# Kernel optimization log

Hardware: AMD Instinct MI355X
Metric: run time of the kernel (lower is better)

## Reference

```python
import jax, jax.numpy as jnp
import numpy as np

H = 64  # hidden_dim


def setup_inputs() -> dict:
    key = jax.random.key(0)
    ks = jax.random.split(key, 6)
    B, S, F = 256, 512, 128
    C = 100
    # small init scale keeps sigmoid/tanh out of saturation (like torch default init)
    return {
        "x": jax.random.normal(ks[0], (B, S, F), dtype=jnp.float32),
        "W_x2h": jax.random.normal(ks[1], (3 * H, F), dtype=jnp.float32) * 0.05,
        "W_h2h": jax.random.normal(ks[2], (3 * H, H), dtype=jnp.float32) * 0.05,
        "W1": jax.random.normal(ks[3], (512, S * H), dtype=jnp.float32) * 0.02,
        "W2": jax.random.normal(ks[4], (256, 512), dtype=jnp.float32) * 0.05,
        "W3": jax.random.normal(ks[5], (C, 256), dtype=jnp.float32) * 0.05,
    }


def reference(x, W_x2h, W_h2h, W1, W2, W3):
    B, S, F = x.shape
    # Precompute input-to-hidden gates for all timesteps in one GEMM: (B,S,3H)
    gx_all = jnp.einsum("bsf,gf->bsg", x, W_x2h)

    def step(h, gx):
        gh = h @ W_h2h.T  # (B, 3H)
        i_r, i_i, i_n = jnp.split(gx, 3, axis=1)
        h_r, h_i, h_n = jnp.split(gh, 3, axis=1)
        resetgate = jax.nn.sigmoid(i_r + h_r)
        inputgate = jax.nn.sigmoid(i_i + h_i)
        newgate = jnp.tanh(i_n + resetgate * h_n)
        h_new = newgate + inputgate * (h - newgate)
        return h_new, h_new

    h0 = jnp.zeros((B, H), dtype=x.dtype)
    _, outs = jax.lax.scan(step, h0, jnp.swapaxes(gx_all, 0, 1))  # outs: (S,B,H)
    out = jnp.swapaxes(outs, 0, 1).reshape(B, S * H)  # stack along dim 1, then flatten

    out = jax.nn.relu(out @ W1.T)
    out = jax.nn.relu(out @ W2.T)
    out = out @ W3.T
    return jax.nn.softmax(out, axis=1)
```

## Files before the change

kernel.cpp:

```cpp
#include <hip/hip_runtime.h>


constexpr int B = 256, S = 512, F = 128, H = 64, G = 192, C = 100;
constexpr int N1 = 512;
constexpr int SCHUNK = 128, NCHUNK = 4;
constexpr int K1 = S * H;

typedef __attribute__((ext_vector_type(8))) __bf16 bf16x8;
typedef __attribute__((ext_vector_type(4))) float f32x4;

__device__ __forceinline__ unsigned short f2bf(float f) {
  unsigned int u = __float_as_uint(f);
  unsigned int r = (u + 0x7FFFu + ((u >> 16) & 1u)) >> 16;
  return (unsigned short)r;
}
__device__ __forceinline__ float bf2f(unsigned short s) {
  return __uint_as_float((unsigned int)s << 16);
}
__device__ __forceinline__ float sigm_fast(float x) {
  float e = __builtin_amdgcn_exp2f(-1.4426950408889634f * x);
  return __builtin_amdgcn_rcpf(1.f + e);
}
__device__ __forceinline__ float tanh_fast(float x) {
  float e = __builtin_amdgcn_exp2f(2.8853900817779268f * x);
  return 1.f - 2.f * __builtin_amdgcn_rcpf(1.f + e);
}
__device__ __forceinline__ float quad_add(float v) {
  int y = __builtin_amdgcn_update_dpp(0, __float_as_int(v), 0xB1, 0xF, 0xF, true);
  float s = v + __int_as_float(y);
  int z = __builtin_amdgcn_update_dpp(0, __float_as_int(s), 0x4E, 0xF, 0xF, true);
  return s + __int_as_float(z);
}

__global__ void k_convW(const float* __restrict__ Wx, unsigned short* __restrict__ Wh_hi,
                        unsigned short* __restrict__ Wh_lo) {
  int el = blockIdx.x * 256 + threadIdx.x;
  float v = Wx[el];
  unsigned short hi = f2bf(v);
  Wh_hi[el] = hi;
  Wh_lo[el] = f2bf(v - bf2f(hi));
}

__global__ __launch_bounds__(256, 1) void k_gemm_gx(const float* __restrict__ x,
                                                    const unsigned short* __restrict__ Whp,
                                                    const unsigned short* __restrict__ Wlp,
                                                    float* __restrict__ gx, int sc) {
  __shared__ unsigned short Ah[128 * 32];
  __shared__ unsigned short Al[128 * 32];
  __shared__ unsigned short Bh[192 * 32];
  __shared__ unsigned short Bl[192 * 32];
  const int t = threadIdx.x;
  const int b = blockIdx.x;
  const int w = t >> 6, l = t & 63;
  const int wm = w >> 1, wn = w & 1;
  const float* arow = x + ((size_t)b * S + (size_t)sc * SCHUNK) * F;

  f32x4 acc[4][6] = {};

  const int ar_ = t >> 1, ahh = t & 1;
  for (int kc = 0; kc < 4; kc++) {
    const int k0 = kc * 32;
    {
      const float* sp = arow + (size_t)ar_ * F + k0 + ahh * 16;
      float fv[16];
#pragma unroll
      for (int c = 0; c < 4; c++) {
        float4 v = *(const float4*)(sp + c * 4);
        fv[c * 4 + 0] = v.x; fv[c * 4 + 1] = v.y; fv[c * 4 + 2] = v.z; fv[c * 4 + 3] = v.w;
      }
      unsigned short hi[16], lo[16];
#pragma unroll
      for (int e = 0; e < 16; e++) {
        hi[e] = f2bf(fv[e]);
        lo[e] = f2bf(fv[e] - bf2f(hi[e]));
      }
#pragma unroll
      for (int half = 0; half < 2; half++) {
        int cq = ahh * 2 + half;
        int sq = cq ^ (ar_ & 3);
        unsigned short* dh = &Ah[ar_ * 32 + sq * 8];
        unsigned short* dl = &Al[ar_ * 32 + sq * 8];
#pragma unroll
        for (int e = 0; e < 8; e++) {
          dh[e] = hi[half * 8 + e];
          dl[e] = lo[half * 8 + e];
        }
      }
    }
    if (t < 192) {
#pragma unroll
      for (int cq = 0; cq < 4; cq++) {
        int sq = cq ^ (t & 3);
        *(uint4*)&Bh[t * 32 + sq * 8] = *(const uint4*)(Whp + (size_t)t * F + k0 + cq * 8);
        *(uint4*)&Bl[t * 32 + sq * 8] = *(const uint4*)(Wlp + (size_t)t * F + k0 + cq * 8);
      }
    }
    __syncthreads();
    bf16x8 bhf[6], blf[6];
#pragma unroll
    for (int nf = 0; nf < 6; nf++) {
      int rowb = wn * 96 + nf * 16 + (l & 15);
      int sq = (l >> 4) ^ (rowb & 3);
      bhf[nf] = *(const bf16x8*)&Bh[rowb * 32 + sq * 8];
      blf[nf] = *(const bf16x8*)&Bl[rowb * 32 + sq * 8];
    }
#pragma unroll
    for (int mf = 0; mf < 4; mf++) {
      int rowa = wm * 64 + mf * 16 + (l & 15);
      int sq = (l >> 4) ^ (rowa & 3);
      bf16x8 ah = *(const bf16x8*)&Ah[rowa * 32 + sq * 8];
      bf16x8 al = *(const bf16x8*)&Al[rowa * 32 + sq * 8];
#pragma unroll
      for (int nf = 0; nf < 6; nf++) {
        acc[mf][nf] = __builtin_amdgcn_mfma_f32_16x16x32_bf16(ah, bhf[nf], acc[mf][nf], 0, 0, 0);
        acc[mf][nf] = __builtin_amdgcn_mfma_f32_16x16x32_bf16(al, bhf[nf], acc[mf][nf], 0, 0, 0);
        acc[mf][nf] = __builtin_amdgcn_mfma_f32_16x16x32_bf16(ah, blf[nf], acc[mf][nf], 0, 0, 0);
      }
    }
    __syncthreads();
  }
#pragma unroll
  for (int mf = 0; mf < 4; mf++) {
#pragma unroll
    for (int nf = 0; nf < 6; nf++) {
      int m = wm * 64 + mf * 16 + (l >> 4) * 4;
      int n = wn * 96 + nf * 16 + (l & 15);
      float* dst = gx + ((size_t)b * SCHUNK + m) * G + n;
#pragma unroll
      for (int r = 0; r < 4; r++) dst[(size_t)r * G] = acc[mf][nf][r];
    }
  }
}

__global__ __launch_bounds__(256, 1) void k_scan(const float* __restrict__ gx,
                                                 const float* __restrict__ Wh,
                                                 unsigned short* __restrict__ outh,
                                                 unsigned short* __restrict__ outl,
                                                 float* __restrict__ hst, int sc) {
  __shared__ float h_s[2][64];
  const int t = threadIdx.x;
  const int w = t >> 6, l = t & 63;
  const int j = (w << 4) | (l >> 2);
  const int q = l & 3;
  const int b = blockIdx.x;

  float Wr[16], Wi[16], Wn[16];
  {
    const float* p0 = Wh + (size_t)j * H + q * 16;
    const float* p1 = Wh + (size_t)(64 + j) * H + q * 16;
    const float* p2 = Wh + (size_t)(128 + j) * H + q * 16;
#pragma unroll
    for (int c = 0; c < 4; c++) {
      float4 v0 = *(const float4*)(p0 + c * 4);
      float4 v1 = *(const float4*)(p1 + c * 4);
      float4 v2 = *(const float4*)(p2 + c * 4);
      Wr[c * 4 + 0] = v0.x; Wr[c * 4 + 1] = v0.y; Wr[c * 4 + 2] = v0.z; Wr[c * 4 + 3] = v0.w;
      Wi[c * 4 + 0] = v1.x; Wi[c * 4 + 1] = v1.y; Wi[c * 4 + 2] = v1.z; Wi[c * 4 + 3] = v1.w;
      Wn[c * 4 + 0] = v2.x; Wn[c * 4 + 1] = v2.y; Wn[c * 4 + 2] = v2.z; Wn[c * 4 + 3] = v2.w;
    }
  }
  float h_own;
  if (sc == 0) {
    h_own = 0.f;
    if (t < 64) h_s[0][t] = 0.f;
  } else {
    h_own = hst[b * H + j];
    if (t < 64) h_s[0][t] = hst[b * H + t];
  }
  asm volatile("s_waitcnt lgkmcnt(0)\n\ts_barrier" ::: "memory");

  const float* gxb = gx + (size_t)b * SCHUNK * G;
  float gr0 = gxb[j], gi0 = gxb[64 + j], gn0 = gxb[128 + j];
  float gr1 = gxb[G + j], gi1 = gxb[G + 64 + j], gn1 = gxb[G + 128 + j];
  unsigned short* poh = outh + (size_t)b * K1 + (size_t)sc * SCHUNK * H + j;
  unsigned short* pol = outl + (size_t)b * K1 + (size_t)sc * SCHUNK * H + j;

  int cur = 0;
  for (int sl = 0; sl < SCHUNK; sl++) {
    const float* hb = &h_s[cur][q * 16];
    float4 ha = *(const float4*)(hb);
    float4 hc = *(const float4*)(hb + 4);
    float4 hd = *(const float4*)(hb + 8);
    float4 he = *(const float4*)(hb + 12);
    int pf = (sl + 2 < SCHUNK) ? sl + 2 : SCHUNK - 1;
    const float* gp = gxb + (size_t)pf * G;
    float grn = gp[j], gin = gp[64 + j], gnn = gp[128 + j];

    float ar, ai, an;
    ar = Wr[0] * ha.x; ai = Wi[0] * ha.x; an = Wn[0] * ha.x;
    ar = fmaf(Wr[1], ha.y, ar); ai = fmaf(Wi[1], ha.y, ai); an = fmaf(Wn[1], ha.y, an);
    ar = fmaf(Wr[2], ha.z, ar); ai = fmaf(Wi[2], ha.z, ai); an = fmaf(Wn[2], ha.z, an);
    ar = fmaf(Wr[3], ha.w, ar); ai = fmaf(Wi[3], ha.w, ai); an = fmaf(Wn[3], ha.w, an);
    ar = fmaf(Wr[4], hc.x, ar); ai = fmaf(Wi[4], hc.x, ai); an = fmaf(Wn[4], hc.x, an);
    ar = fmaf(Wr[5], hc.y, ar); ai = fmaf(Wi[5], hc.y, ai); an = fmaf(Wn[5], hc.y, an);
    ar = fmaf(Wr[6], hc.z, ar); ai = fmaf(Wi[6], hc.z, ai); an = fmaf(Wn[6], hc.z, an);
    ar = fmaf(Wr[7], hc.w, ar); ai = fmaf(Wi[7], hc.w, ai); an = fmaf(Wn[7], hc.w, an);
    ar = fmaf(Wr[8], hd.x, ar); ai = fmaf(Wi[8], hd.x, ai); an = fmaf(Wn[8], hd.x, an);
    ar = fmaf(Wr[9], hd.y, ar); ai = fmaf(Wi[9], hd.y, ai); an = fmaf(Wn[9], hd.y, an);
    ar = fmaf(Wr[10], hd.z, ar); ai = fmaf(Wi[10], hd.z, ai); an = fmaf(Wn[10], hd.z, an);
    ar = fmaf(Wr[11], hd.w, ar); ai = fmaf(Wi[11], hd.w, ai); an = fmaf(Wn[11], hd.w, an);
    ar = fmaf(Wr[12], he.x, ar); ai = fmaf(Wi[12], he.x, ai); an = fmaf(Wn[12], he.x, an);
    ar = fmaf(Wr[13], he.y, ar); ai = fmaf(Wi[13], he.y, ai); an = fmaf(Wn[13], he.y, an);
    ar = fmaf(Wr[14], he.z, ar); ai = fmaf(Wi[14], he.z, ai); an = fmaf(Wn[14], he.z, an);
    ar = fmaf(Wr[15], he.w, ar); ai = fmaf(Wi[15], he.w, ai); an = fmaf(Wn[15], he.w, an);

    ar = quad_add(ar);
    ai = quad_add(ai);
    an = quad_add(an);

    float rr = sigm_fast(ar + gr0);
    float ii = sigm_fast(ai + gi0);
    float na = gn0 + rr * an;
    float th = tanh_fast(na);
    h_own = th + ii * (h_own - th);

    int nxt = cur ^ 1;
    if (q == 0) {
      h_s[nxt][j] = h_own;
      unsigned short hh2 = f2bf(h_own);
      poh[(size_t)sl * H] = hh2;
      pol[(size_t)sl * H] = f2bf(h_own - bf2f(hh2));
    }
    gr0 = gr1; gi0 = gi1; gn0 = gn1;
    gr1 = grn; gi1 = gin; gn1 = gnn;
    asm volatile("s_waitcnt lgkmcnt(0)\n\ts_barrier" ::: "memory");
    cur = nxt;
  }
  if (q == 0) hst[b * H + j] = h_own;
}

__global__ __launch_bounds__(256, 1) void k_fc1(const unsigned short* __restrict__ Ahp,
                                                const unsigned short* __restrict__ Alp,
                                                const float* __restrict__ W1,
                                                float* __restrict__ psum, int KCH) {
  __shared__ unsigned short Ah[256 * 32];
  __shared__ unsigned short Al[256 * 32];
  __shared__ unsigned short Bh[128 * 32];
  __shared__ unsigned short Bl[128 * 32];
  const int t = threadIdx.x;
  const int ntile = blockIdx.x & 3;
  const int ks = blockIdx.x >> 2;
  const int k0b = ks * KCH;
  const int w = t >> 6, l = t & 63;
  const int wm = w >> 1, wn = w & 1;

  f32x4 acc[8][4] = {};

  const int br = t >> 1, bhh = t & 1;
  const float* bsrc = W1 + (size_t)(ntile * 128 + br) * K1 + bhh * 16;
  const int nkc = KCH >> 5;

  for (int kc = 0; kc < nkc; kc++) {
    const int k0 = k0b + kc * 32;
#pragma unroll
    for (int i = 0; i < 4; i++) {
      int slot = t + i * 256;
      int row = slot >> 2, sq = slot & 3;
      int cq = sq ^ (row & 3);
      const uint4* sh = (const uint4*)(Ahp + (size_t)row * K1 + k0 + cq * 8);
      const uint4* sl2 = (const uint4*)(Alp + (size_t)row * K1 + k0 + cq * 8);
      *(uint4*)&Ah[row * 32 + sq * 8] = *sh;
      *(uint4*)&Al[row * 32 + sq * 8] = *sl2;
    }
    {
      const float* sp = bsrc + k0;
      float fv[16];
#pragma unroll
      for (int c = 0; c < 4; c++) {
        float4 v = *(const float4*)(sp + c * 4);
        fv[c * 4 + 0] = v.x; fv[c * 4 + 1] = v.y; fv[c * 4 + 2] = v.z; fv[c * 4 + 3] = v.w;
      }
      unsigned short hi[16], lo[16];
#pragma unroll
      for (int e = 0; e < 16; e++) {
        hi[e] = f2bf(fv[e]);
        lo[e] = f2bf(fv[e] - bf2f(hi[e]));
      }
#pragma unroll
      for (int half = 0; half < 2; half++) {
        int cq = bhh * 2 + half;
        int sq = cq ^ (br & 3);
        unsigned short* dh = &Bh[br * 32 + sq * 8];
        unsigned short* dl = &Bl[br * 32 + sq * 8];
#pragma unroll
        for (int e = 0; e < 8; e++) {
          dh[e] = hi[half * 8 + e];
          dl[e] = lo[half * 8 + e];
        }
      }
    }
    __syncthreads();
    bf16x8 bhf[4], blf[4];
#pragma unroll
    for (int nf = 0; nf < 4; nf++) {
      int rowb = wn * 64 + nf * 16 + (l & 15);
      int sq = (l >> 4) ^ (rowb & 3);
      bhf[nf] = *(const bf16x8*)&Bh[rowb * 32 + sq * 8];
      blf[nf] = *(const bf16x8*)&Bl[rowb * 32 + sq * 8];
    }
#pragma unroll
    for (int mf = 0; mf < 8; mf++) {
      int rowa = wm * 128 + mf * 16 + (l & 15);
      int sq = (l >> 4) ^ (rowa & 3);
      bf16x8 ah = *(const bf16x8*)&Ah[rowa * 32 + sq * 8];
      bf16x8 al = *(const bf16x8*)&Al[rowa * 32 + sq * 8];
#pragma unroll
      for (int nf = 0; nf < 4; nf++) {
        acc[mf][nf] = __builtin_amdgcn_mfma_f32_16x16x32_bf16(ah, bhf[nf], acc[mf][nf], 0, 0, 0);
        acc[mf][nf] = __builtin_amdgcn_mfma_f32_16x16x32_bf16(al, bhf[nf], acc[mf][nf], 0, 0, 0);
        acc[mf][nf] = __builtin_amdgcn_mfma_f32_16x16x32_bf16(ah, blf[nf], acc[mf][nf], 0, 0, 0);
      }
    }
    __syncthreads();
  }
#pragma unroll
  for (int mf = 0; mf < 8; mf++) {
#pragma unroll
    for (int nf = 0; nf < 4; nf++) {
      int m = wm * 128 + mf * 16 + (l >> 4) * 4;
      int n = ntile * 128 + wn * 64 + nf * 16 + (l & 15);
      float* dst = psum + ((size_t)ks * 256 + m) * N1 + n;
#pragma unroll
      for (int r = 0; r < 4; r++) dst[(size_t)r * N1] = acc[mf][nf][r];
    }
  }
}

__global__ void k_red(const float* __restrict__ psum, float* __restrict__ out1, int KS) {
  int i = (blockIdx.x * 256 + threadIdx.x) * 4;
  float4 s = make_float4(0.f, 0.f, 0.f, 0.f);
  for (int ks = 0; ks < KS; ks++) {
    float4 v = *(const float4*)(psum + (size_t)ks * (B * N1) + i);
    s.x += v.x; s.y += v.y; s.z += v.z; s.w += v.w;
  }
  *(float4*)(out1 + i) = s;
}

__global__ __launch_bounds__(256, 1) void k_tail(const float* __restrict__ out1,
                                                 const float* __restrict__ W2,
                                                 const float* __restrict__ W3,
                                                 float* __restrict__ dout) {
  __shared__ float o1[N1];
  __shared__ float o2[256];
  __shared__ float lg[128];
  const int tid = threadIdx.x;
  const int b = blockIdx.x;
  {
    float2 v = *(const float2*)(out1 + (size_t)b * N1 + tid * 2);
    o1[tid * 2 + 0] = fmaxf(v.x, 0.f);
    o1[tid * 2 + 1] = fmaxf(v.y, 0.f);
  }
  __syncthreads();
  {
    const float* w2r = W2 + (size_t)tid * N1;
    float a0 = 0, a1 = 0, a2 = 0, a3 = 0;
#pragma unroll 4
    for (int k = 0; k < N1; k += 4) {
      float4 ov = *(const float4*)(o1 + k);
      float4 wv = *(const float4*)(w2r + k);
      a0 = fmaf(ov.x, wv.x, a0);
      a1 = fmaf(ov.y, wv.y, a1);
      a2 = fmaf(ov.z, wv.z, a2);
      a3 = fmaf(ov.w, wv.w, a3);
    }
    o2[tid] = fmaxf((a0 + a1) + (a2 + a3), 0.f);
  }
  __syncthreads();
  if (tid < C) {
    const float* w3r = W3 + (size_t)tid * 256;
    float a0 = 0, a1 = 0, a2 = 0, a3 = 0;
#pragma unroll 4
    for (int k = 0; k < 256; k += 4) {
      float4 ov = *(const float4*)(o2 + k);
      float4 wv = *(const float4*)(w3r + k);
      a0 = fmaf(ov.x, wv.x, a0);
      a1 = fmaf(ov.y, wv.y, a1);
      a2 = fmaf(ov.z, wv.z, a2);
      a3 = fmaf(ov.w, wv.w, a3);
    }
    lg[tid] = (a0 + a1) + (a2 + a3);
  }
  __syncthreads();
  if (tid < 64) {
    float v0 = lg[tid];
    float v1 = (tid + 64 < C) ? lg[tid + 64] : -3.0e38f;
    float m = fmaxf(v0, v1);
#pragma unroll
    for (int off = 32; off > 0; off >>= 1) m = fmaxf(m, __shfl_xor(m, off, 64));
    float e0 = __expf(v0 - m);
    float e1 = (tid + 64 < C) ? __expf(v1 - m) : 0.f;
    float ssum = e0 + e1;
#pragma unroll
    for (int off = 32; off > 0; off >>= 1) ssum += __shfl_xor(ssum, off, 64);
    float inv = 1.f / ssum;
    dout[(size_t)b * C + tid] = e0 * inv;
    if (tid + 64 < C) dout[(size_t)b * C + tid + 64] = e1 * inv;
  }
}

extern "C" void kernel_launch(void* const* d_in, const int* in_sizes, int n_in,
                              void* d_out, int out_size, void* d_ws, size_t ws_size,
                              hipStream_t stream) {
  (void)in_sizes; (void)n_in; (void)out_size;
  const float* x = (const float*)d_in[0];
  const float* Wx = (const float*)d_in[1];
  const float* Wh = (const float*)d_in[2];
  const float* W1 = (const float*)d_in[3];
  const float* W2 = (const float*)d_in[4];
  const float* W3 = (const float*)d_in[5];
  float* ws = (float*)d_ws;

  const int KS = (ws_size >= 110ull * 1024 * 1024) ? 64 : 32;
  const int KCH = K1 / KS;

  const size_t gx_f = (size_t)B * SCHUNK * G;
  const size_t psum_f = (size_t)KS * B * N1;
  const size_t region0 = (psum_f > gx_f) ? psum_f : gx_f;

  float* gx = ws;
  float* psum = ws;
  unsigned short* gouth = (unsigned short*)(ws + region0);
  unsigned short* goutl = gouth + (size_t)B * K1;
  float* out1 = (float*)(goutl + (size_t)B * K1);
  float* hst = out1 + (size_t)B * N1;
  unsigned short* Wxh = (unsigned short*)(hst + (size_t)B * H);
  unsigned short* Wxl = Wxh + (size_t)G * F;

  k_convW<<<dim3((G * F) / 256), dim3(256), 0, stream>>>(Wx, Wxh, Wxl);
  for (int sc = 0; sc < NCHUNK; sc++) {
    k_gemm_gx<<<dim3(B), dim3(256), 0, stream>>>(x, Wxh, Wxl, gx, sc);
    k_scan<<<dim3(B), dim3(256), 0, stream>>>(gx, Wh, gouth, goutl, hst, sc);
  }
  k_fc1<<<dim3(4 * KS), dim3(256), 0, stream>>>(gouth, goutl, W1, psum, KCH);
  k_red<<<dim3(128), dim3(256), 0, stream>>>(psum, out1, KS);
  k_tail<<<dim3(B), dim3(256), 0, stream>>>(out1, W2, W3, (float*)d_out);
}
```

Baseline: 488.9 us.

## Fuse input GEMM into GRU scan kernel and use atomic split-K for FC1

The per-chunk input-projection GEMM and the recurrent scan are merged into one persistent kernel. Each block computes its gate pre-activations into a shared-memory buffer of about 96 KB and then runs the scan over all four chunks. This drops eight launches, the global gx round trip and the hidden-state save and restore between chunks. FC1 moves to 512-thread blocks with a fixed split-K of 64 and a block-index swizzle, and it accumulates with atomicAdd into a zeroed output instead of writing partial sums and running a separate reduction. In exchange the scan block needs a large LDS allocation, loads the A and B operands straight from global memory without staging, and the FC1 result becomes order-nondeterministic.

```diff
diff --git a/kernel.cpp b/kernel.cpp
--- a/kernel.cpp
+++ b/kernel.cpp
@@ -7,7 +7,13 @@
 constexpr int K1 = S * H;
 
 typedef __attribute__((ext_vector_type(8))) __bf16 bf16x8;
+typedef __attribute__((ext_vector_type(8))) short s16x8;
 typedef __attribute__((ext_vector_type(4))) float f32x4;
+
+union BFU {
+  s16x8 s;
+  bf16x8 b;
+};
 
 __device__ __forceinline__ unsigned short f2bf(float f) {
   unsigned int u = __float_as_uint(f);
@@ -41,110 +47,23 @@
   Wh_lo[el] = f2bf(v - bf2f(hi));
 }
 
-__global__ __launch_bounds__(256, 1) void k_gemm_gx(const float* __restrict__ x,
-                                                    const unsigned short* __restrict__ Whp,
-                                                    const unsigned short* __restrict__ Wlp,
-                                                    float* __restrict__ gx, int sc) {
-  __shared__ unsigned short Ah[128 * 32];
-  __shared__ unsigned short Al[128 * 32];
-  __shared__ unsigned short Bh[192 * 32];
-  __shared__ unsigned short Bl[192 * 32];
-  const int t = threadIdx.x;
-  const int b = blockIdx.x;
-  const int w = t >> 6, l = t & 63;
-  const int wm = w >> 1, wn = w & 1;
-  const float* arow = x + ((size_t)b * S + (size_t)sc * SCHUNK) * F;
-
-  f32x4 acc[4][6] = {};
-
-  const int ar_ = t >> 1, ahh = t & 1;
-  for (int kc = 0; kc < 4; kc++) {
-    const int k0 = kc * 32;
-    {
-      const float* sp = arow + (size_t)ar_ * F + k0 + ahh * 16;
-      float fv[16];
-#pragma unroll
-      for (int c = 0; c < 4; c++) {
-        float4 v = *(const float4*)(sp + c * 4);
-        fv[c * 4 + 0] = v.x; fv[c * 4 + 1] = v.y; fv[c * 4 + 2] = v.z; fv[c * 4 + 3] = v.w;
-      }
-      unsigned short hi[16], lo[16];
-#pragma unroll
-      for (int e = 0; e < 16; e++) {
-        hi[e] = f2bf(fv[e]);
-        lo[e] = f2bf(fv[e] - bf2f(hi[e]));
-      }
-#pragma unroll
-      for (int half = 0; half < 2; half++) {
-        int cq = ahh * 2 + half;
-        int sq = cq ^ (ar_ & 3);
-        unsigned short* dh = &Ah[ar_ * 32 + sq * 8];
-        unsigned short* dl = &Al[ar_ * 32 + sq * 8];
-#pragma unroll
-        for (int e = 0; e < 8; e++) {
-          dh[e] = hi[half * 8 + e];
-          dl[e] = lo[half * 8 + e];
-        }
-      }
-    }
-    if (t < 192) {
-#pragma unroll
-      for (int cq = 0; cq < 4; cq++) {
-        int sq = cq ^ (t & 3);
-        *(uint4*)&Bh[t * 32 + sq * 8] = *(const uint4*)(Whp + (size_t)t * F + k0 + cq * 8);
-        *(uint4*)&Bl[t * 32 + sq * 8] = *(const uint4*)(Wlp + (size_t)t * F + k0 + cq * 8);
-      }
-    }
-    __syncthreads();
-    bf16x8 bhf[6], blf[6];
-#pragma unroll
-    for (int nf = 0; nf < 6; nf++) {
-      int rowb = wn * 96 + nf * 16 + (l & 15);
-      int sq = (l >> 4) ^ (rowb & 3);
-      bhf[nf] = *(const bf16x8*)&Bh[rowb * 32 + sq * 8];
-      blf[nf] = *(const bf16x8*)&Bl[rowb * 32 + sq * 8];
-    }
-#pragma unroll
-    for (int mf = 0; mf < 4; mf++) {
-      int rowa = wm * 64 + mf * 16 + (l & 15);
-      int sq = (l >> 4) ^ (rowa & 3);
-      bf16x8 ah = *(const bf16x8*)&Ah[rowa * 32 + sq * 8];
-      bf16x8 al = *(const bf16x8*)&Al[rowa * 32 + sq * 8];
-#pragma unroll
-      for (int nf = 0; nf < 6; nf++) {
-        acc[mf][nf] = __builtin_amdgcn_mfma_f32_16x16x32_bf16(ah, bhf[nf], acc[mf][nf], 0, 0, 0);
-        acc[mf][nf] = __builtin_amdgcn_mfma_f32_16x16x32_bf16(al, bhf[nf], acc[mf][nf], 0, 0, 0);
-        acc[mf][nf] = __builtin_amdgcn_mfma_f32_16x16x32_bf16(ah, blf[nf], acc[mf][nf], 0, 0, 0);
-      }
-    }
-    __syncthreads();
-  }
-#pragma unroll
-  for (int mf = 0; mf < 4; mf++) {
-#pragma unroll
-    for (int nf = 0; nf < 6; nf++) {
-      int m = wm * 64 + mf * 16 + (l >> 4) * 4;
-      int n = wn * 96 + nf * 16 + (l & 15);
-      float* dst = gx + ((size_t)b * SCHUNK + m) * G + n;
-#pragma unroll
-      for (int r = 0; r < 4; r++) dst[(size_t)r * G] = acc[mf][nf][r];
-    }
-  }
-}
-
-__global__ __launch_bounds__(256, 1) void k_scan(const float* __restrict__ gx,
-                                                 const float* __restrict__ Wh,
-                                                 unsigned short* __restrict__ outh,
-                                                 unsigned short* __restrict__ outl,
-                                                 float* __restrict__ hst, int sc) {
+__global__ __launch_bounds__(256, 1) void k_fused(const float* __restrict__ x,
+                                                  const unsigned short* __restrict__ Whp,
+                                                  const unsigned short* __restrict__ Wlp,
+                                                  const float* __restrict__ Wh,
+                                                  unsigned short* __restrict__ outh,
+                                                  unsigned short* __restrict__ outl) {
+  __shared__ float gxl[SCHUNK * G];
   __shared__ float h_s[2][64];
   const int t = threadIdx.x;
   const int w = t >> 6, l = t & 63;
+  const int b = blockIdx.x;
+  const int wm = w >> 1, wn = w & 1;
+  const int lm = l & 15, lk = l >> 4;
   const int j = (w << 4) | (l >> 2);
   const int q = l & 3;
-  const int b = blockIdx.x;
-
-  float Wr[16], Wi[16], Wn[16];
+
+  float Wr[16], Wi[16], Wn_[16];
   {
     const float* p0 = Wh + (size_t)j * H + q * 16;
     const float* p1 = Wh + (size_t)(64 + j) * H + q * 16;
@@ -156,152 +75,179 @@
       float4 v2 = *(const float4*)(p2 + c * 4);
       Wr[c * 4 + 0] = v0.x; Wr[c * 4 + 1] = v0.y; Wr[c * 4 + 2] = v0.z; Wr[c * 4 + 3] = v0.w;
       Wi[c * 4 + 0] = v1.x; Wi[c * 4 + 1] = v1.y; Wi[c * 4 + 2] = v1.z; Wi[c * 4 + 3] = v1.w;
-      Wn[c * 4 + 0] = v2.x; Wn[c * 4 + 1] = v2.y; Wn[c * 4 + 2] = v2.z; Wn[c * 4 + 3] = v2.w;
-    }
-  }
-  float h_own;
-  if (sc == 0) {
-    h_own = 0.f;
-    if (t < 64) h_s[0][t] = 0.f;
-  } else {
-    h_own = hst[b * H + j];
-    if (t < 64) h_s[0][t] = hst[b * H + t];
-  }
-  asm volatile("s_waitcnt lgkmcnt(0)\n\ts_barrier" ::: "memory");
-
-  const float* gxb = gx + (size_t)b * SCHUNK * G;
-  float gr0 = gxb[j], gi0 = gxb[64 + j], gn0 = gxb[128 + j];
-  float gr1 = gxb[G + j], gi1 = gxb[G + 64 + j], gn1 = gxb[G + 128 + j];
-  unsigned short* poh = outh + (size_t)b * K1 + (size_t)sc * SCHUNK * H + j;
-  unsigned short* pol = outl + (size_t)b * K1 + (size_t)sc * SCHUNK * H + j;
-
+      Wn_[c * 4 + 0] = v2.x; Wn_[c * 4 + 1] = v2.y; Wn_[c * 4 + 2] = v2.z; Wn_[c * 4 + 3] = v2.w;
+    }
+  }
+  float h_own = 0.f;
+  if (t < 64) h_s[0][t] = 0.f;
   int cur = 0;
-  for (int sl = 0; sl < SCHUNK; sl++) {
-    const float* hb = &h_s[cur][q * 16];
-    float4 ha = *(const float4*)(hb);
-    float4 hc = *(const float4*)(hb + 4);
-    float4 hd = *(const float4*)(hb + 8);
-    float4 he = *(const float4*)(hb + 12);
-    int pf = (sl + 2 < SCHUNK) ? sl + 2 : SCHUNK - 1;
-    const float* gp = gxb + (size_t)pf * G;
-    float grn = gp[j], gin = gp[64 + j], gnn = gp[128 + j];
-
-    float ar, ai, an;
-    ar = Wr[0] * ha.x; ai = Wi[0] * ha.x; an = Wn[0] * ha.x;
-    ar = fmaf(Wr[1], ha.y, ar); ai = fmaf(Wi[1], ha.y, ai); an = fmaf(Wn[1], ha.y, an);
-    ar = fmaf(Wr[2], ha.z, ar); ai = fmaf(Wi[2], ha.z, ai); an = fmaf(Wn[2], ha.z, an);
-    ar = fmaf(Wr[3], ha.w, ar); ai = fmaf(Wi[3], ha.w, ai); an = fmaf(Wn[3], ha.w, an);
-    ar = fmaf(Wr[4], hc.x, ar); ai = fmaf(Wi[4], hc.x, ai); an = fmaf(Wn[4], hc.x, an);
-    ar = fmaf(Wr[5], hc.y, ar); ai = fmaf(Wi[5], hc.y, ai); an = fmaf(Wn[5], hc.y, an);
-    ar = fmaf(Wr[6], hc.z, ar); ai = fmaf(Wi[6], hc.z, ai); an = fmaf(Wn[6], hc.z, an);
-    ar = fmaf(Wr[7], hc.w, ar); ai = fmaf(Wi[7], hc.w, ai); an = fmaf(Wn[7], hc.w, an);
-    ar = fmaf(Wr[8], hd.x, ar); ai = fmaf(Wi[8], hd.x, ai); an = fmaf(Wn[8], hd.x, an);
-    ar = fmaf(Wr[9], hd.y, ar); ai = fmaf(Wi[9], hd.y, ai); an = fmaf(Wn[9], hd.y, an);
-    ar = fmaf(Wr[10], hd.z, ar); ai = fmaf(Wi[10], hd.z, ai); an = fmaf(Wn[10], hd.z, an);
-    ar = fmaf(Wr[11], hd.w, ar); ai = fmaf(Wi[11], hd.w, ai); an = fmaf(Wn[11], hd.w, an);
-    ar = fmaf(Wr[12], he.x, ar); ai = fmaf(Wi[12], he.x, ai); an = fmaf(Wn[12], he.x, an);
-    ar = fmaf(Wr[13], he.y, ar); ai = fmaf(Wi[13], he.y, ai); an = fmaf(Wn[13], he.y, an);
-    ar = fmaf(Wr[14], he.z, ar); ai = fmaf(Wi[14], he.z, ai); an = fmaf(Wn[14], he.z, an);
-    ar = fmaf(Wr[15], he.w, ar); ai = fmaf(Wi[15], he.w, ai); an = fmaf(Wn[15], he.w, an);
-
-    ar = quad_add(ar);
-    ai = quad_add(ai);
-    an = quad_add(an);
-
-    float rr = sigm_fast(ar + gr0);
-    float ii = sigm_fast(ai + gi0);
-    float na = gn0 + rr * an;
-    float th = tanh_fast(na);
-    h_own = th + ii * (h_own - th);
-
-    int nxt = cur ^ 1;
-    if (q == 0) {
-      h_s[nxt][j] = h_own;
-      unsigned short hh2 = f2bf(h_own);
-      poh[(size_t)sl * H] = hh2;
-      pol[(size_t)sl * H] = f2bf(h_own - bf2f(hh2));
-    }
-    gr0 = gr1; gi0 = gi1; gn0 = gn1;
-    gr1 = grn; gi1 = gin; gn1 = gnn;
-    asm volatile("s_waitcnt lgkmcnt(0)\n\ts_barrier" ::: "memory");
-    cur = nxt;
-  }
-  if (q == 0) hst[b * H + j] = h_own;
-}
-
-__global__ __launch_bounds__(256, 1) void k_fc1(const unsigned short* __restrict__ Ahp,
+  __syncthreads();
+
+  unsigned short* poh_b = outh + (size_t)b * K1 + j;
+  unsigned short* pol_b = outl + (size_t)b * K1 + j;
+
+  for (int sc = 0; sc < NCHUNK; sc++) {
+    const float* arow = x + ((size_t)b * S + (size_t)sc * SCHUNK) * F;
+    f32x4 acc[4][6] = {};
+#pragma unroll
+    for (int kc = 0; kc < 4; kc++) {
+      const int k0 = kc * 32;
+      bf16x8 bhf[6], blf[6];
+#pragma unroll
+      for (int nf = 0; nf < 6; nf++) {
+        int g = wn * 96 + nf * 16 + lm;
+        bhf[nf] = *(const bf16x8*)(Whp + (size_t)g * F + k0 + lk * 8);
+        blf[nf] = *(const bf16x8*)(Wlp + (size_t)g * F + k0 + lk * 8);
+      }
+#pragma unroll
+      for (int mf = 0; mf < 4; mf++) {
+        int rowa = wm * 64 + mf * 16 + lm;
+        const float* ap = arow + (size_t)rowa * F + k0 + lk * 8;
+        float4 a0 = *(const float4*)(ap);
+        float4 a1 = *(const float4*)(ap + 4);
+        float av[8] = {a0.x, a0.y, a0.z, a0.w, a1.x, a1.y, a1.z, a1.w};
+        BFU ah, al;
+#pragma unroll
+        for (int e = 0; e < 8; e++) {
+          unsigned short hi = f2bf(av[e]);
+          ah.s[e] = (short)hi;
+          al.s[e] = (short)f2bf(av[e] - bf2f(hi));
+        }
+#pragma unroll
+        for (int nf = 0; nf < 6; nf++) {
+          acc[mf][nf] = __builtin_amdgcn_mfma_f32_16x16x32_bf16(ah.b, bhf[nf], acc[mf][nf], 0, 0, 0);
+          acc[mf][nf] = __builtin_amdgcn_mfma_f32_16x16x32_bf16(al.b, bhf[nf], acc[mf][nf], 0, 0, 0);
+          acc[mf][nf] = __builtin_amdgcn_mfma_f32_16x16x32_bf16(ah.b, blf[nf], acc[mf][nf], 0, 0, 0);
+        }
+      }
+    }
+#pragma unroll
+    for (int mf = 0; mf < 4; mf++)
+#pragma unroll
+      for (int nf = 0; nf < 6; nf++) {
+        int m = wm * 64 + mf * 16 + lk * 4;
+        int n = wn * 96 + nf * 16 + lm;
+#pragma unroll
+        for (int r = 0; r < 4; r++) gxl[(m + r) * G + n] = acc[mf][nf][r];
+      }
+    __syncthreads();
+
+    float gr = gxl[j], gi = gxl[64 + j], gn = gxl[128 + j];
+    for (int sl = 0; sl < SCHUNK; sl++) {
+      const float* hb = &h_s[cur][q * 16];
+      float4 ha = *(const float4*)(hb);
+      float4 hc = *(const float4*)(hb + 4);
+      float4 hd = *(const float4*)(hb + 8);
+      float4 he = *(const float4*)(hb + 12);
+      int np = (sl + 1) & (SCHUNK - 1);
+      float grn = gxl[np * G + j];
+      float gin = gxl[np * G + 64 + j];
+      float gnn = gxl[np * G + 128 + j];
+
+      float ar, ai, an;
+      ar = Wr[0] * ha.x; ai = Wi[0] * ha.x; an = Wn_[0] * ha.x;
+      ar = fmaf(Wr[1], ha.y, ar); ai = fmaf(Wi[1], ha.y, ai); an = fmaf(Wn_[1], ha.y, an);
+      ar = fmaf(Wr[2], ha.z, ar); ai = fmaf(Wi[2], ha.z, ai); an = fmaf(Wn_[2], ha.z, an);
+      ar = fmaf(Wr[3], ha.w, ar); ai = fmaf(Wi[3], ha.w, ai); an = fmaf(Wn_[3], ha.w, an);
+      ar = fmaf(Wr[4], hc.x, ar); ai = fmaf(Wi[4], hc.x, ai); an = fmaf(Wn_[4], hc.x, an);
+      ar = fmaf(Wr[5], hc.y, ar); ai = fmaf(Wi[5], hc.y, ai); an = fmaf(Wn_[5], hc.y, an);
+      ar = fmaf(Wr[6], hc.z, ar); ai = fmaf(Wi[6], hc.z, ai); an = fmaf(Wn_[6], hc.z, an);
+      ar = fmaf(Wr[7], hc.w, ar); ai = fmaf(Wi[7], hc.w, ai); an = fmaf(Wn_[7], hc.w, an);
+      ar = fmaf(Wr[8], hd.x, ar); ai = fmaf(Wi[8], hd.x, ai); an = fmaf(Wn_[8], hd.x, an);
+      ar = fmaf(Wr[9], hd.y, ar); ai = fmaf(Wi[9], hd.y, ai); an = fmaf(Wn_[9], hd.y, an);
+      ar = fmaf(Wr[10], hd.z, ar); ai = fmaf(Wi[10], hd.z, ai); an = fmaf(Wn_[10], hd.z, an);
+      ar = fmaf(Wr[11], hd.w, ar); ai = fmaf(Wi[11], hd.w, ai); an = fmaf(Wn_[11], hd.w, an);
+      ar = fmaf(Wr[12], he.x, ar); ai = fmaf(Wi[12], he.x, ai); an = fmaf(Wn_[12], he.x, an);
+      ar = fmaf(Wr[13], he.y, ar); ai = fmaf(Wi[13], he.y, ai); an = fmaf(Wn_[13], he.y, an);
+      ar = fmaf(Wr[14], he.z, ar); ai = fmaf(Wi[14], he.z, ai); an = fmaf(Wn_[14], he.z, an);
+      ar = fmaf(Wr[15], he.w, ar); ai = fmaf(Wi[15], he.w, ai); an = fmaf(Wn_[15], he.w, an);
+
+      ar = quad_add(ar);
+      ai = quad_add(ai);
+      an = quad_add(an);
+
+      float rr = sigm_fast(ar + gr);
+      float ii = sigm_fast(ai + gi);
+      float na = gn + rr * an;
+      float th = tanh_fast(na);
+      h_own = th + ii * (h_own - th);
+
+      int nxt = cur ^ 1;
+      if (q == 0) {
+        h_s[nxt][j] = h_own;
+        unsigned short hh = f2bf(h_own);
+        size_t so = (size_t)(sc * SCHUNK + sl) * H;
+        poh_b[so] = hh;
+        pol_b[so] = f2bf(h_own - bf2f(hh));
+      }
+      gr = grn; gi = gin; gn = gnn;
+      asm volatile("s_waitcnt lgkmcnt(0)\n\ts_barrier" ::: "memory");
+      cur = nxt;
+    }
+  }
+}
+
+__global__ __launch_bounds__(512, 1) void k_fc1(const unsigned short* __restrict__ Ahp,
                                                 const unsigned short* __restrict__ Alp,
                                                 const float* __restrict__ W1,
-                                                float* __restrict__ psum, int KCH) {
+                                                float* __restrict__ out1) {
   __shared__ unsigned short Ah[256 * 32];
   __shared__ unsigned short Al[256 * 32];
   __shared__ unsigned short Bh[128 * 32];
   __shared__ unsigned short Bl[128 * 32];
   const int t = threadIdx.x;
-  const int ntile = blockIdx.x & 3;
-  const int ks = blockIdx.x >> 2;
-  const int k0b = ks * KCH;
+  const int bid = blockIdx.x;
+  const int v = (bid & 7) * 32 + (bid >> 3);
+  const int ks = v >> 2, ntile = v & 3;
+  const int k0b = ks * 512;
   const int w = t >> 6, l = t & 63;
   const int wm = w >> 1, wn = w & 1;
-
-  f32x4 acc[8][4] = {};
-
-  const int br = t >> 1, bhh = t & 1;
-  const float* bsrc = W1 + (size_t)(ntile * 128 + br) * K1 + bhh * 16;
-  const int nkc = KCH >> 5;
-
-  for (int kc = 0; kc < nkc; kc++) {
+  const int lm = l & 15, lk = l >> 4;
+
+  f32x4 acc[4][4] = {};
+  const int br = t >> 2, qt = t & 3;
+
+  for (int kc = 0; kc < 16; kc++) {
     const int k0 = k0b + kc * 32;
 #pragma unroll
-    for (int i = 0; i < 4; i++) {
-      int slot = t + i * 256;
+    for (int i = 0; i < 2; i++) {
+      int slot = t + i * 512;
       int row = slot >> 2, sq = slot & 3;
       int cq = sq ^ (row & 3);
-      const uint4* sh = (const uint4*)(Ahp + (size_t)row * K1 + k0 + cq * 8);
-      const uint4* sl2 = (const uint4*)(Alp + (size_t)row * K1 + k0 + cq * 8);
-      *(uint4*)&Ah[row * 32 + sq * 8] = *sh;
-      *(uint4*)&Al[row * 32 + sq * 8] = *sl2;
+      *(uint4*)&Ah[row * 32 + sq * 8] = *(const uint4*)(Ahp + (size_t)row * K1 + k0 + cq * 8);
+      *(uint4*)&Al[row * 32 + sq * 8] = *(const uint4*)(Alp + (size_t)row * K1 + k0 + cq * 8);
     }
     {
-      const float* sp = bsrc + k0;
-      float fv[16];
-#pragma unroll
-      for (int c = 0; c < 4; c++) {
-        float4 v = *(const float4*)(sp + c * 4);
-        fv[c * 4 + 0] = v.x; fv[c * 4 + 1] = v.y; fv[c * 4 + 2] = v.z; fv[c * 4 + 3] = v.w;
-      }
-      unsigned short hi[16], lo[16];
-#pragma unroll
-      for (int e = 0; e < 16; e++) {
-        hi[e] = f2bf(fv[e]);
-        lo[e] = f2bf(fv[e] - bf2f(hi[e]));
-      }
-#pragma unroll
-      for (int half = 0; half < 2; half++) {
-        int cq = bhh * 2 + half;
-        int sq = cq ^ (br & 3);
-        unsigned short* dh = &Bh[br * 32 + sq * 8];
-        unsigned short* dl = &Bl[br * 32 + sq * 8];
-#pragma unroll
-        for (int e = 0; e < 8; e++) {
-          dh[e] = hi[half * 8 + e];
-          dl[e] = lo[half * 8 + e];
-        }
-      }
+      const float* sp = W1 + (size_t)(ntile * 128 + br) * K1 + k0 + qt * 8;
+      float4 v0 = *(const float4*)(sp);
+      float4 v1 = *(const float4*)(sp + 4);
+      float fv[8] = {v0.x, v0.y, v0.z, v0.w, v1.x, v1.y, v1.z, v1.w};
+      unsigned int hp[4], lp[4];
+#pragma unroll
+      for (int e = 0; e < 4; e++) {
+        unsigned short h0 = f2bf(fv[2 * e]), h1 = f2bf(fv[2 * e + 1]);
+        unsigned short l0 = f2bf(fv[2 * e] - bf2f(h0));
+        unsigned short l1 = f2bf(fv[2 * e + 1] - bf2f(h1));
+        hp[e] = (unsigned int)h0 | ((unsigned int)h1 << 16);
+        lp[e] = (unsigned int)l0 | ((unsigned int)l1 << 16);
+      }
+      int sq = qt ^ (br & 3);
+      *(uint4*)&Bh[br * 32 + sq * 8] = make_uint4(hp[0], hp[1], hp[2], hp[3]);
+      *(uint4*)&Bl[br * 32 + sq * 8] = make_uint4(lp[0], lp[1], lp[2], lp[3]);
     }
     __syncthreads();
     bf16x8 bhf[4], blf[4];
 #pragma unroll
     for (int nf = 0; nf < 4; nf++) {
-      int rowb = wn * 64 + nf * 16 + (l & 15);
-      int sq = (l >> 4) ^ (rowb & 3);
+      int rowb = wn * 64 + nf * 16 + lm;
+      int sq = lk ^ (rowb & 3);
       bhf[nf] = *(const bf16x8*)&Bh[rowb * 32 + sq * 8];
       blf[nf] = *(const bf16x8*)&Bl[rowb * 32 + sq * 8];
     }
 #pragma unroll
-    for (int mf = 0; mf < 8; mf++) {
-      int rowa = wm * 128 + mf * 16 + (l & 15);
-      int sq = (l >> 4) ^ (rowa & 3);
+    for (int mf = 0; mf < 4; mf++) {
+      int rowa = wm * 64 + mf * 16 + lm;
+      int sq = lk ^ (rowa & 3);
       bf16x8 ah = *(const bf16x8*)&Ah[rowa * 32 + sq * 8];
       bf16x8 al = *(const bf16x8*)&Al[rowa * 32 + sq * 8];
 #pragma unroll
@@ -314,26 +260,15 @@
     __syncthreads();
   }
 #pragma unroll
-  for (int mf = 0; mf < 8; mf++) {
+  for (int mf = 0; mf < 4; mf++)
 #pragma unroll
     for (int nf = 0; nf < 4; nf++) {
-      int m = wm * 128 + mf * 16 + (l >> 4) * 4;
-      int n = ntile * 128 + wn * 64 + nf * 16 + (l & 15);
-      float* dst = psum + ((size_t)ks * 256 + m) * N1 + n;
-#pragma unroll
-      for (int r = 0; r < 4; r++) dst[(size_t)r * N1] = acc[mf][nf][r];
-    }
-  }
-}
-
-__global__ void k_red(const float* __restrict__ psum, float* __restrict__ out1, int KS) {
-  int i = (blockIdx.x * 256 + threadIdx.x) * 4;
-  float4 s = make_float4(0.f, 0.f, 0.f, 0.f);
-  for (int ks = 0; ks < KS; ks++) {
-    float4 v = *(const float4*)(psum + (size_t)ks * (B * N1) + i);
-    s.x += v.x; s.y += v.y; s.z += v.z; s.w += v.w;
-  }
-  *(float4*)(out1 + i) = s;
+      int m = wm * 64 + mf * 16 + lk * 4;
+      int n = ntile * 128 + wn * 64 + nf * 16 + lm;
+#pragma unroll
+      for (int r = 0; r < 4; r++)
+        atomicAdd(out1 + (size_t)(m + r) * N1 + n, acc[mf][nf][r]);
+    }
 }
 
 __global__ __launch_bounds__(256, 1) void k_tail(const float* __restrict__ out1,
@@ -401,37 +336,23 @@
 extern "C" void kernel_launch(void* const* d_in, const int* in_sizes, int n_in,
                               void* d_out, int out_size, void* d_ws, size_t ws_size,
                               hipStream_t stream) {
-  (void)in_sizes; (void)n_in; (void)out_size;
+  (void)in_sizes; (void)n_in; (void)out_size; (void)ws_size;
   const float* x = (const float*)d_in[0];
   const float* Wx = (const float*)d_in[1];
   const float* Wh = (const float*)d_in[2];
   const float* W1 = (const float*)d_in[3];
   const float* W2 = (const float*)d_in[4];
   const float* W3 = (const float*)d_in[5];
-  float* ws = (float*)d_ws;
-
-  const int KS = (ws_size >= 110ull * 1024 * 1024) ? 64 : 32;
-  const int KCH = K1 / KS;
-
-  const size_t gx_f = (size_t)B * SCHUNK * G;
-  const size_t psum_f = (size_t)KS * B * N1;
-  const size_t region0 = (psum_f > gx_f) ? psum_f : gx_f;
-
-  float* gx = ws;
-  float* psum = ws;
-  unsigned short* gouth = (unsigned short*)(ws + region0);
+
+  unsigned short* Wxh = (unsigned short*)d_ws;
+  unsigned short* Wxl = Wxh + (size_t)G * F;
+  unsigned short* gouth = Wxl + (size_t)G * F;
   unsigned short* goutl = gouth + (size_t)B * K1;
   float* out1 = (float*)(goutl + (size_t)B * K1);
-  float* hst = out1 + (size_t)B * N1;
-  unsigned short* Wxh = (unsigned short*)(hst + (size_t)B * H);
-  unsigned short* Wxl = Wxh + (size_t)G * F;
-
+
+  hipMemsetAsync(out1, 0, (size_t)B * N1 * sizeof(float), stream);
   k_convW<<<dim3((G * F) / 256), dim3(256), 0, stream>>>(Wx, Wxh, Wxl);
-  for (int sc = 0; sc < NCHUNK; sc++) {
-    k_gemm_gx<<<dim3(B), dim3(256), 0, stream>>>(x, Wxh, Wxl, gx, sc);
-    k_scan<<<dim3(B), dim3(256), 0, stream>>>(gx, Wh, gouth, goutl, hst, sc);
-  }
-  k_fc1<<<dim3(4 * KS), dim3(256), 0, stream>>>(gouth, goutl, W1, psum, KCH);
-  k_red<<<dim3(128), dim3(256), 0, stream>>>(psum, out1, KS);
+  k_fused<<<dim3(B), dim3(256), 0, stream>>>(x, Wxh, Wxl, Wh, gouth, goutl);
+  k_fc1<<<dim3(256), dim3(512), 0, stream>>>(gouth, goutl, W1, out1);
   k_tail<<<dim3(B), dim3(256), 0, stream>>>(out1, W2, W3, (float*)d_out);
 }
```

After: 423.6 us. 1.15x faster.
